# Optimization experiments

Hardware: AMD Instinct MI355X
Metric: run time of the kernel (lower is better)

Reference implementation:

```python
import jax, jax.numpy as jnp
import numpy as np
from jax import lax

B = 32768
IMG = 28  # MNIST image side
K = 3     # conv kernel side
OUT_HW = IMG - K + 1  # 26 -> 676 flattened


def setup_inputs() -> dict:
    key = jax.random.key(0)
    ks = jax.random.split(key, 6)
    return {
        "x": jax.random.normal(ks[0], (B, IMG * IMG), dtype=jnp.float32),
        "conv_w": jax.random.normal(ks[1], (K, K), dtype=jnp.float32),
        "w0": jax.random.normal(ks[2], (200, OUT_HW * OUT_HW), dtype=jnp.float32) * 0.04,
        "b0": jax.random.normal(ks[3], (200,), dtype=jnp.float32) * 0.01,
        "w1": jax.random.normal(ks[4], (10, 200), dtype=jnp.float32) * 0.07,
        "b1": jax.random.normal(ks[5], (10,), dtype=jnp.float32) * 0.01,
    }


def reference(x, conv_w, w0, b0, w1, b1):
    # Valid 2D cross-correlation (matches the torch tensordot patch loop)
    xi = x.reshape(-1, 1, IMG, IMG)              # [B,1,28,28]
    kern = conv_w[None, None, :, :]              # [1,1,3,3]
    y = lax.conv_general_dilated(
        xi, kern, window_strides=(1, 1), padding="VALID",
        dimension_numbers=("NCHW", "OIHW", "NCHW"))  # [B,1,26,26]
    flat = y.reshape(y.shape[0], OUT_HW * OUT_HW)    # [B,676]
    h = jax.nn.relu(flat @ w0.T + b0)                # [B,200]
    return h @ w1.T + b1                             # [B,10] logits
```

## Files before the change

kernel.cpp:

```cpp
#include <hip/hip_runtime.h>
#include <hip/hip_bf16.h>

#define IMG 28
#define OHW 26
#define NPIX (OHW * OHW)
#define KPAD 704
#define NH 200
#define NHPAD 224
#define NOUT 10
#define MT 32
#define ASTRIDE 712
#define HSTRIDE 208

typedef __attribute__((ext_vector_type(8))) short bf16x8;
typedef __attribute__((ext_vector_type(4))) float f32x4;

static __device__ __forceinline__ unsigned short bf16_bits(float v) {
    __hip_bfloat16 b = __float2bfloat16(v);
    return *(unsigned short*)&b;
}

__global__ void cast_w0_kernel(const float* __restrict__ w0,
                               __hip_bfloat16* __restrict__ w0b) {
    int idx = blockIdx.x * blockDim.x + threadIdx.x;
    if (idx >= NHPAD * KPAD) return;
    int n = idx / KPAD;
    int k = idx - n * KPAD;
    float v = (n < NH && k < NPIX) ? w0[n * NPIX + k] : 0.0f;
    w0b[idx] = __float2bfloat16(v);
}

template <int NT>
static __device__ __forceinline__ void fc0_loop(
    const __hip_bfloat16* __restrict__ a0,
    const __hip_bfloat16* __restrict__ a1,
    const __hip_bfloat16* __restrict__ bbase,
    f32x4 acc[2][4])
{
    for (int k0 = 0; k0 < KPAD; k0 += 32) {
        bf16x8 af0 = *(const bf16x8*)(a0 + k0);
        bf16x8 af1 = *(const bf16x8*)(a1 + k0);
#pragma unroll
        for (int t = 0; t < NT; ++t) {
            bf16x8 bf = *(const bf16x8*)(bbase + (size_t)t * 16 * KPAD + k0);
            acc[0][t] = __builtin_amdgcn_mfma_f32_16x16x32_bf16(af0, bf, acc[0][t], 0, 0, 0);
            acc[1][t] = __builtin_amdgcn_mfma_f32_16x16x32_bf16(af1, bf, acc[1][t], 0, 0, 0);
        }
    }
}

__global__ __launch_bounds__(256, 3) void fused_mlp_kernel(
    const float* __restrict__ x,
    const float* __restrict__ cw,
    const __hip_bfloat16* __restrict__ w0b,
    const float* __restrict__ b0,
    const float* __restrict__ w1,
    const float* __restrict__ b1,
    float* __restrict__ out)
{
    __shared__ __align__(16) char lds_raw[MT * ASTRIDE * 2];
    __hip_bfloat16* A = (__hip_bfloat16*)lds_raw;
    float* H = (float*)lds_raw;

    const int tid = threadIdx.x;
    const int img0 = blockIdx.x * MT;

    const float k00 = cw[0], k01 = cw[1], k02 = cw[2];
    const float k10 = cw[3], k11 = cw[4], k12 = cw[5];
    const float k20 = cw[6], k21 = cw[7], k22 = cw[8];

    for (int idx = tid; idx < MT * (ASTRIDE - NPIX); idx += 256) {
        int i = idx / (ASTRIDE - NPIX);
        int c = idx - i * (ASTRIDE - NPIX);
        ((unsigned short*)A)[i * ASTRIDE + NPIX + c] = 0;
    }

    for (int task = tid; task < MT * OHW; task += 256) {
        int img  = task / OHW;
        int orow = task - img * OHW;
        const float* base = x + (size_t)(img0 + img) * (IMG * IMG) + orow * IMG;

        float4 r0[7], r1[7], r2[7];
#pragma unroll
        for (int j = 0; j < 7; ++j) {
            r0[j] = ((const float4*)base)[j];
            r1[j] = ((const float4*)(base + IMG))[j];
            r2[j] = ((const float4*)(base + 2 * IMG))[j];
        }
        const float* a0r = (const float*)r0;
        const float* a1r = (const float*)r1;
        const float* a2r = (const float*)r2;

        unsigned short obits[OHW];
#pragma unroll
        for (int c = 0; c < OHW; ++c) {
            float acc = a0r[c] * k00 + a0r[c + 1] * k01 + a0r[c + 2] * k02
                      + a1r[c] * k10 + a1r[c + 1] * k11 + a1r[c + 2] * k12
                      + a2r[c] * k20 + a2r[c + 1] * k21 + a2r[c + 2] * k22;
            obits[c] = bf16_bits(acc);
        }
        unsigned* dst = (unsigned*)(A + img * ASTRIDE + orow * OHW);
#pragma unroll
        for (int c2 = 0; c2 < 13; ++c2) {
            dst[c2] = (unsigned)obits[2 * c2] | ((unsigned)obits[2 * c2 + 1] << 16);
        }
    }
    __syncthreads();

    const int wave = tid >> 6;
    const int lane = tid & 63;
    const int lm   = lane & 15;
    const int quad = lane >> 4;
    const int ntbase = (wave < 2) ? wave * 4 : 8 + (wave - 2) * 3;
    const int ntn    = (wave < 2) ? 4 : 3;

    f32x4 acc[2][4];
#pragma unroll
    for (int m = 0; m < 2; ++m)
#pragma unroll
        for (int t = 0; t < 4; ++t) acc[m][t] = (f32x4){0.f, 0.f, 0.f, 0.f};

    {
        const __hip_bfloat16* a0 = A + (0 * 16 + lm) * ASTRIDE + quad * 8;
        const __hip_bfloat16* a1 = A + (1 * 16 + lm) * ASTRIDE + quad * 8;
        const __hip_bfloat16* bb = w0b + (size_t)(ntbase * 16 + lm) * KPAD + quad * 8;
        if (wave < 2) fc0_loop<4>(a0, a1, bb, acc);
        else          fc0_loop<3>(a0, a1, bb, acc);
    }
    __syncthreads();

#pragma unroll
    for (int t = 0; t < 4; ++t) {
        if (t < ntn) {
            int n = (ntbase + t) * 16 + lm;
            if (n < NH) {
                float bv = b0[n];
#pragma unroll
                for (int m = 0; m < 2; ++m) {
#pragma unroll
                    for (int r = 0; r < 4; ++r) {
                        int mm = m * 16 + quad * 4 + r;
                        float v = acc[m][t][r] + bv;
                        H[mm * HSTRIDE + n] = v > 0.f ? v : 0.f;
                    }
                }
            }
        }
    }
    __syncthreads();

    for (int idx = tid; idx < MT * NOUT; idx += 256) {
        int i = idx / NOUT;
        int j = idx - i * NOUT;
        const float4* hrow = (const float4*)(H + i * HSTRIDE);
        const float4* wrow = (const float4*)(w1 + j * NH);
        float s = b1[j];
        float4 accv = {0.f, 0.f, 0.f, 0.f};
#pragma unroll 5
        for (int n = 0; n < NH / 4; ++n) {
            float4 h4 = hrow[n];
            float4 w4 = wrow[n];
            accv.x += h4.x * w4.x;
            accv.y += h4.y * w4.y;
            accv.z += h4.z * w4.z;
            accv.w += h4.w * w4.w;
        }
        s += (accv.x + accv.y) + (accv.z + accv.w);
        out[(size_t)(img0 + i) * NOUT + j] = s;
    }
}

extern "C" void kernel_launch(void* const* d_in, const int* in_sizes, int n_in,
                              void* d_out, int out_size, void* d_ws, size_t ws_size,
                              hipStream_t stream) {
    const float* x   = (const float*)d_in[0];
    const float* cw  = (const float*)d_in[1];
    const float* w0  = (const float*)d_in[2];
    const float* b0  = (const float*)d_in[3];
    const float* w1  = (const float*)d_in[4];
    const float* b1  = (const float*)d_in[5];
    float* out = (float*)d_out;

    __hip_bfloat16* w0b = (__hip_bfloat16*)d_ws;

    int cast_elems = NHPAD * KPAD;
    cast_w0_kernel<<<(cast_elems + 255) / 256, 256, 0, stream>>>(w0, w0b);

    int nblocks = 32768 / MT;
    fused_mlp_kernel<<<nblocks, 256, 0, stream>>>(x, cw, w0b, b0, w1, b1, out);
}
```

Measured before the change: 208.7 us.

## Pre-pack w0 into MFMA fragment order and split N tiles across 8 waves

Measured after the change: 202.0 us. 3.2% less time.

```diff
diff --git a/kernel.cpp b/kernel.cpp
--- a/kernel.cpp
+++ b/kernel.cpp
@@ -3,10 +3,10 @@
 
 #define IMG 28
 #define OHW 26
-#define NPIX (OHW * OHW)
-#define KPAD 704
+#define NPIX 676
+#define KT_N 22
+#define NT_N 13
 #define NH 200
-#define NHPAD 224
 #define NOUT 10
 #define MT 32
 #define ASTRIDE 712
@@ -20,39 +20,20 @@
     return *(unsigned short*)&b;
 }
 
-__global__ void cast_w0_kernel(const float* __restrict__ w0,
-                               __hip_bfloat16* __restrict__ w0b) {
+__global__ void pack_weights(const float* __restrict__ w0,
+                             __hip_bfloat16* __restrict__ Bf) {
     int idx = blockIdx.x * blockDim.x + threadIdx.x;
-    if (idx >= NHPAD * KPAD) return;
-    int n = idx / KPAD;
-    int k = idx - n * KPAD;
-    float v = (n < NH && k < NPIX) ? w0[n * NPIX + k] : 0.0f;
-    w0b[idx] = __float2bfloat16(v);
+    if (idx >= NT_N * KT_N * 512) return;
+    int j = idx & 7, L = (idx >> 3) & 63, kt = (idx >> 9) % KT_N, nt = idx / (KT_N * 512);
+    int n = nt * 16 + (L & 15), k = kt * 32 + ((L >> 4) << 3) + j;
+    float v = (n < NH && k < NPIX) ? w0[n * NPIX + k] : 0.f;
+    Bf[idx] = __float2bfloat16(v);
 }
 
-template <int NT>
-static __device__ __forceinline__ void fc0_loop(
-    const __hip_bfloat16* __restrict__ a0,
-    const __hip_bfloat16* __restrict__ a1,
-    const __hip_bfloat16* __restrict__ bbase,
-    f32x4 acc[2][4])
-{
-    for (int k0 = 0; k0 < KPAD; k0 += 32) {
-        bf16x8 af0 = *(const bf16x8*)(a0 + k0);
-        bf16x8 af1 = *(const bf16x8*)(a1 + k0);
-#pragma unroll
-        for (int t = 0; t < NT; ++t) {
-            bf16x8 bf = *(const bf16x8*)(bbase + (size_t)t * 16 * KPAD + k0);
-            acc[0][t] = __builtin_amdgcn_mfma_f32_16x16x32_bf16(af0, bf, acc[0][t], 0, 0, 0);
-            acc[1][t] = __builtin_amdgcn_mfma_f32_16x16x32_bf16(af1, bf, acc[1][t], 0, 0, 0);
-        }
-    }
-}
-
-__global__ __launch_bounds__(256, 3) void fused_mlp_kernel(
+__global__ __launch_bounds__(512, 6) void fused_mlp_kernel(
     const float* __restrict__ x,
     const float* __restrict__ cw,
-    const __hip_bfloat16* __restrict__ w0b,
+    const __hip_bfloat16* __restrict__ Bf,
     const float* __restrict__ b0,
     const float* __restrict__ w1,
     const float* __restrict__ b1,
@@ -69,13 +50,13 @@
     const float k10 = cw[3], k11 = cw[4], k12 = cw[5];
     const float k20 = cw[6], k21 = cw[7], k22 = cw[8];
 
-    for (int idx = tid; idx < MT * (ASTRIDE - NPIX); idx += 256) {
+    for (int idx = tid; idx < MT * (ASTRIDE - NPIX); idx += 512) {
         int i = idx / (ASTRIDE - NPIX);
         int c = idx - i * (ASTRIDE - NPIX);
         ((unsigned short*)A)[i * ASTRIDE + NPIX + c] = 0;
     }
 
-    for (int task = tid; task < MT * OHW; task += 256) {
+    for (int task = tid; task < MT * OHW; task += 512) {
         int img  = task / OHW;
         int orow = task - img * OHW;
         const float* base = x + (size_t)(img0 + img) * (IMG * IMG) + orow * IMG;
@@ -110,27 +91,46 @@
     const int wave = tid >> 6;
     const int lane = tid & 63;
     const int lm   = lane & 15;
-    const int quad = lane >> 4;
-    const int ntbase = (wave < 2) ? wave * 4 : 8 + (wave - 2) * 3;
-    const int ntn    = (wave < 2) ? 4 : 3;
+    const int q    = lane >> 4;
+    const int ntbase = (wave < 5) ? wave * 2 : 10 + (wave - 5);
+    const int ntn    = (wave < 5) ? 2 : 1;
 
-    f32x4 acc[2][4];
+    f32x4 acc[2][2];
 #pragma unroll
     for (int m = 0; m < 2; ++m)
 #pragma unroll
-        for (int t = 0; t < 4; ++t) acc[m][t] = (f32x4){0.f, 0.f, 0.f, 0.f};
+        for (int t = 0; t < 2; ++t) acc[m][t] = (f32x4){0.f, 0.f, 0.f, 0.f};
 
     {
-        const __hip_bfloat16* a0 = A + (0 * 16 + lm) * ASTRIDE + quad * 8;
-        const __hip_bfloat16* a1 = A + (1 * 16 + lm) * ASTRIDE + quad * 8;
-        const __hip_bfloat16* bb = w0b + (size_t)(ntbase * 16 + lm) * KPAD + quad * 8;
-        if (wave < 2) fc0_loop<4>(a0, a1, bb, acc);
-        else          fc0_loop<3>(a0, a1, bb, acc);
+        const __hip_bfloat16* a0 = A + lm * ASTRIDE + q * 8;
+        const __hip_bfloat16* a1 = A + (16 + lm) * ASTRIDE + q * 8;
+        const bf16x8* bb = (const bf16x8*)Bf + (size_t)ntbase * KT_N * 64 + lane;
+
+        if (ntn == 2) {
+            for (int kt = 0; kt < KT_N; ++kt) {
+                bf16x8 af0 = *(const bf16x8*)(a0 + kt * 32);
+                bf16x8 af1 = *(const bf16x8*)(a1 + kt * 32);
+                bf16x8 bf0 = bb[kt * 64];
+                bf16x8 bf1 = bb[(KT_N + kt) * 64];
+                acc[0][0] = __builtin_amdgcn_mfma_f32_16x16x32_bf16(af0, bf0, acc[0][0], 0, 0, 0);
+                acc[1][0] = __builtin_amdgcn_mfma_f32_16x16x32_bf16(af1, bf0, acc[1][0], 0, 0, 0);
+                acc[0][1] = __builtin_amdgcn_mfma_f32_16x16x32_bf16(af0, bf1, acc[0][1], 0, 0, 0);
+                acc[1][1] = __builtin_amdgcn_mfma_f32_16x16x32_bf16(af1, bf1, acc[1][1], 0, 0, 0);
+            }
+        } else {
+            for (int kt = 0; kt < KT_N; ++kt) {
+                bf16x8 af0 = *(const bf16x8*)(a0 + kt * 32);
+                bf16x8 af1 = *(const bf16x8*)(a1 + kt * 32);
+                bf16x8 bf0 = bb[kt * 64];
+                acc[0][0] = __builtin_amdgcn_mfma_f32_16x16x32_bf16(af0, bf0, acc[0][0], 0, 0, 0);
+                acc[1][0] = __builtin_amdgcn_mfma_f32_16x16x32_bf16(af1, bf0, acc[1][0], 0, 0, 0);
+            }
+        }
     }
     __syncthreads();
 
 #pragma unroll
-    for (int t = 0; t < 4; ++t) {
+    for (int t = 0; t < 2; ++t) {
         if (t < ntn) {
             int n = (ntbase + t) * 16 + lm;
             if (n < NH) {
@@ -139,7 +139,7 @@
                 for (int m = 0; m < 2; ++m) {
 #pragma unroll
                     for (int r = 0; r < 4; ++r) {
-                        int mm = m * 16 + quad * 4 + r;
+                        int mm = m * 16 + q * 4 + r;
                         float v = acc[m][t][r] + bv;
                         H[mm * HSTRIDE + n] = v > 0.f ? v : 0.f;
                     }
@@ -149,14 +149,14 @@
     }
     __syncthreads();
 
-    for (int idx = tid; idx < MT * NOUT; idx += 256) {
-        int i = idx / NOUT;
-        int j = idx - i * NOUT;
+    if (tid < MT * NOUT) {
+        int i = tid / NOUT;
+        int j = tid - i * NOUT;
         const float4* hrow = (const float4*)(H + i * HSTRIDE);
         const float4* wrow = (const float4*)(w1 + j * NH);
         float s = b1[j];
         float4 accv = {0.f, 0.f, 0.f, 0.f};
-#pragma unroll 5
+#pragma unroll 10
         for (int n = 0; n < NH / 4; ++n) {
             float4 h4 = hrow[n];
             float4 w4 = wrow[n];
@@ -181,11 +181,10 @@
     const float* b1  = (const float*)d_in[5];
     float* out = (float*)d_out;
 
-    __hip_bfloat16* w0b = (__hip_bfloat16*)d_ws;
+    __hip_bfloat16* Bf = (__hip_bfloat16*)d_ws;
 
-    int cast_elems = NHPAD * KPAD;
-    cast_w0_kernel<<<(cast_elems + 255) / 256, 256, 0, stream>>>(w0, w0b);
+    const int pack_elems = NT_N * KT_N * 512;
+    pack_weights<<<(pack_elems + 255) / 256, 256, 0, stream>>>(w0, Bf);
 
-    int nblocks = 32768 / MT;
-    fused_mlp_kernel<<<nblocks, 256, 0, stream>>>(x, cw, w0b, b0, w1, b1, out);
+    fused_mlp_kernel<<<32768 / MT, 512, 0, stream>>>(x, cw, Bf, b0, w1, b1, out);
 }
```
